# Kernel optimization log

Hardware: AMD Instinct MI355X
Metric: run time of the kernel (lower is better)

The kernel has to match this reference:

```python
import jax, jax.numpy as jnp
import numpy as np
import math

B, S, D, H, L, F = 32, 512, 512, 8, 4, 1024
TD = 4 * D  # time embedding dim
DH = D // H
SCALE = 1.0 / math.sqrt(DH)


def _ln(x, g, b):
    m = jnp.mean(x, -1, keepdims=True)
    v = jnp.var(x, -1, keepdims=True)
    return (x - m) * jax.lax.rsqrt(v + 1e-5) * g + b


def setup_inputs() -> dict:
    key = jax.random.key(0)
    ks = jax.random.split(key, 12)
    w = lambda k, shp: jax.random.normal(k, shp, dtype=jnp.float32) * 0.02
    return {
        "x": jax.random.normal(ks[0], (B, S, D), dtype=jnp.float32),
        "time": jax.random.uniform(ks[1], (B,), dtype=jnp.float32) * 1000.0,
        "time_w1": w(ks[2], (TD, D)), "time_b1": jnp.zeros((TD,), jnp.float32),
        "time_w2": w(ks[3], (TD, TD)), "time_b2": jnp.zeros((TD,), jnp.float32),
        "Wq": w(ks[4], (L, D, D)), "bq": jnp.zeros((L, D), jnp.float32),
        "Wk": w(ks[5], (L, D, D)), "bk": jnp.zeros((L, D), jnp.float32),
        "Wv": w(ks[6], (L, D, D)), "bv": jnp.zeros((L, D), jnp.float32),
        "Wo": w(ks[7], (L, D, D)), "bo": jnp.zeros((L, D), jnp.float32),
        "attn_g": jnp.ones((L, D), jnp.float32), "attn_b": jnp.zeros((L, D), jnp.float32),
        "ffn_g": jnp.ones((L, D), jnp.float32), "ffn_b": jnp.zeros((L, D), jnp.float32),
        "W1": w(ks[8], (L, 2 * F, D)), "b1": jnp.zeros((L, 2 * F), jnp.float32),
        "W2": w(ks[9], (L, D, F)), "b2": jnp.zeros((L, D), jnp.float32),
        "Wt": w(ks[10], (L, 4 * F, TD)), "bt": jnp.zeros((L, 4 * F), jnp.float32),
        "head_g": jnp.ones((D,), jnp.float32), "head_b": jnp.zeros((D,), jnp.float32),
        "Wh": w(ks[11], (D, D)), "bh": jnp.zeros((D,), jnp.float32),
    }


def _forward(x, time, time_w1, time_b1, time_w2, time_b2,
             Wq, bq, Wk, bk, Wv, bv, Wo, bo,
             attn_g, attn_b, ffn_g, ffn_b,
             W1, b1, W2, b2, Wt, bt,
             head_g, head_b, Wh, bh):
    Bsz = x.shape[0]
    # --- sinusoidal time embedding + time MLP ---
    half = D // 2
    freqs = jnp.exp(jnp.arange(half, dtype=jnp.float32) * (-math.log(10000.0) / (half - 1)))
    e = time[:, None] * freqs[None, :]
    temb = jnp.concatenate([jnp.sin(e), jnp.cos(e)], axis=-1)  # [B, D]
    temb = jax.nn.gelu(temb @ time_w1.T + time_b1, approximate=False) @ time_w2.T + time_b2  # [B, 4D]
    for i in range(L):
        # attention (prenorm; block 0 skips the norm since first_prenormalization=False)
        h = x if i == 0 else _ln(x, attn_g[i], attn_b[i])
        q = (h @ Wq[i].T + bq[i]).reshape(Bsz, S, H, DH)
        k = (h @ Wk[i].T + bk[i]).reshape(Bsz, S, H, DH)
        v = (h @ Wv[i].T + bv[i]).reshape(Bsz, S, H, DH)
        logits = jnp.einsum('bqhd,bkhd->bhqk', q, k) * SCALE
        probs = jax.nn.softmax(logits, axis=-1)
        o = jnp.einsum('bhqk,bkhd->bqhd', probs, v).reshape(Bsz, S, D)
        x = x + (o @ Wo[i].T + bo[i])
        # FFN with FiLM time conditioning and ReGLU activation
        h = _ln(x, ffn_g[i], ffn_b[i])
        h1 = h @ W1[i].T + b1[i]  # [B, S, 2F]
        tm = jax.nn.silu(temb) @ Wt[i].T + bt[i]  # [B, 4F]
        scale, shift = jnp.split(tm[:, None, :], 2, axis=-1)  # each [B, 1, 2F]
        h1 = h1 * (scale + 1.0) + shift
        a, g = jnp.split(h1, 2, axis=-1)  # ReGLU: a * relu(g)
        x = x + ((a * jax.nn.relu(g)) @ W2[i].T + b2[i])
    # head: last token -> LayerNorm -> ReLU -> Linear
    z = _ln(x[:, -1], head_g, head_b)
    return jax.nn.relu(z) @ Wh.T + bh


def reference(x, time, time_w1, time_b1, time_w2, time_b2,
              Wq, bq, Wk, bk, Wv, bv, Wo, bo,
              attn_g, attn_b, ffn_g, ffn_b,
              W1, b1, W2, b2, Wt, bt,
              head_g, head_b, Wh, bh):
    return _forward(x, time, time_w1, time_b1, time_w2, time_b2,
                    Wq, bq, Wk, bk, Wv, bv, Wo, bo,
                    attn_g, attn_b, ffn_g, ffn_b,
                    W1, b1, W2, b2, Wt, bt,
                    head_g, head_b, Wh, bh)
```

## Files before the change

### kernel.cpp

```cpp
#include <hip/hip_runtime.h>
#include <math.h>

typedef __bf16 bf16_t;
typedef __bf16 bf16x8 __attribute__((ext_vector_type(8)));
typedef float f32x4 __attribute__((ext_vector_type(4)));

__device__ __forceinline__ void gload_lds16(const void* g, void* l) {
    __builtin_amdgcn_global_load_lds(
        (const __attribute__((address_space(1))) void*)g,
        (__attribute__((address_space(3))) void*)l, 16, 0, 0);
}

__global__ void k_f2b(const float* __restrict__ in, bf16_t* __restrict__ out, int n8) {
    int idx = blockIdx.x * 256 + threadIdx.x;
    if (idx >= n8) return;
    const float* p = in + (size_t)idx * 8;
    bf16x8 r;
#pragma unroll
    for (int j = 0; j < 8; j++) r[j] = (bf16_t)p[j];
    *(bf16x8*)(out + (size_t)idx * 8) = r;
}

__global__ void k_f2b_s(const float* __restrict__ in, bf16_t* __restrict__ out,
                        int seg8, int dstride8) {
    int idx = blockIdx.x * 256 + threadIdx.x;
    int seg = idx / seg8, rem = idx - seg * seg8;
    const float* p = in + (size_t)idx * 8;
    bf16x8 r;
#pragma unroll
    for (int j = 0; j < 8; j++) r[j] = (bf16_t)p[j];
    *(bf16x8*)(out + ((size_t)seg * dstride8 + rem) * 8) = r;
}

__global__ void k_time_embed(const float* __restrict__ time, float* __restrict__ temb0) {
    int b = blockIdx.x;
    int j = threadIdx.x;
    float f = __expf((float)j * -0.036118981458730134f);
    float e = time[b] * f;
    temb0[(size_t)b * 512 + j] = sinf(e);
    temb0[(size_t)b * 512 + 256 + j] = cosf(e);
}

template<bool DO_NORM>
__global__ void k_ln(const float* __restrict__ x, const float* __restrict__ g,
                     const float* __restrict__ b, bf16_t* __restrict__ out) {
    int row = blockIdx.x * 4 + (threadIdx.x >> 6);
    int lane = threadIdx.x & 63;
    const float* xr = x + (size_t)row * 512 + lane * 8;
    float4 v0 = *(const float4*)xr;
    float4 v1 = *(const float4*)(xr + 4);
    float vals[8] = {v0.x, v0.y, v0.z, v0.w, v1.x, v1.y, v1.z, v1.w};
    bf16x8 r;
    if (DO_NORM) {
        float s = 0.f, sq = 0.f;
#pragma unroll
        for (int j = 0; j < 8; j++) { s += vals[j]; sq += vals[j] * vals[j]; }
#pragma unroll
        for (int m = 1; m < 64; m <<= 1) { s += __shfl_xor(s, m, 64); sq += __shfl_xor(sq, m, 64); }
        float mean = s * (1.0f / 512.0f);
        float var = sq * (1.0f / 512.0f) - mean * mean;
        float rstd = rsqrtf(var + 1e-5f);
        float4 g0 = *(const float4*)(g + lane * 8);
        float4 g1 = *(const float4*)(g + lane * 8 + 4);
        float4 b0 = *(const float4*)(b + lane * 8);
        float4 b1 = *(const float4*)(b + lane * 8 + 4);
        float gs[8] = {g0.x, g0.y, g0.z, g0.w, g1.x, g1.y, g1.z, g1.w};
        float bs[8] = {b0.x, b0.y, b0.z, b0.w, b1.x, b1.y, b1.z, b1.w};
#pragma unroll
        for (int j = 0; j < 8; j++) r[j] = (bf16_t)((vals[j] - mean) * rstd * gs[j] + bs[j]);
    } else {
#pragma unroll
        for (int j = 0; j < 8; j++) r[j] = (bf16_t)vals[j];
    }
    *(bf16x8*)(out + (size_t)row * 512 + lane * 8) = r;
}

__global__ void k_head_prep(const float* __restrict__ x, const float* __restrict__ g,
                            const float* __restrict__ b, float* __restrict__ z) {
    int row = blockIdx.x * 4 + (threadIdx.x >> 6);
    int lane = threadIdx.x & 63;
    const float* xr = x + ((size_t)row * 512 + 511) * 512 + lane * 8;
    float4 v0 = *(const float4*)xr;
    float4 v1 = *(const float4*)(xr + 4);
    float vals[8] = {v0.x, v0.y, v0.z, v0.w, v1.x, v1.y, v1.z, v1.w};
    float s = 0.f, sq = 0.f;
#pragma unroll
    for (int j = 0; j < 8; j++) { s += vals[j]; sq += vals[j] * vals[j]; }
#pragma unroll
    for (int m = 1; m < 64; m <<= 1) { s += __shfl_xor(s, m, 64); sq += __shfl_xor(sq, m, 64); }
    float mean = s * (1.0f / 512.0f);
    float var = sq * (1.0f / 512.0f) - mean * mean;
    float rstd = rsqrtf(var + 1e-5f);
    float o[8];
#pragma unroll
    for (int j = 0; j < 8; j++) {
        float gv = g[lane * 8 + j], bv = b[lane * 8 + j];
        o[j] = fmaxf((vals[j] - mean) * rstd * gv + bv, 0.0f);
    }
    float* zr = z + (size_t)row * 512 + lane * 8;
    *(float4*)zr = make_float4(o[0], o[1], o[2], o[3]);
    *(float4*)(zr + 4) = make_float4(o[4], o[5], o[6], o[7]);
}

template<int ACT, int K, bool OUTB>
__global__ __launch_bounds__(256, 2)
void k_gemm_tm(const float* __restrict__ A, const float* __restrict__ W,
               const float* __restrict__ bias, void* __restrict__ outp, int N) {
    __shared__ float Asm[32][516];
    const int t = threadIdx.x;
    const int kq = t & 7, rw = (t >> 3) & 7, bh = t >> 6;
    const int n0 = blockIdx.x * 32;
    float acc[4][8] = {};
    for (int k0 = 0; k0 < K; k0 += 512) {
        __syncthreads();
#pragma unroll
        for (int i = 0; i < 16; i++) {
            int fid = t + i * 256;
            int row = fid >> 7, cc = (fid & 127) << 2;
            *(float4*)&Asm[row][cc] = *(const float4*)&A[(size_t)row * K + k0 + cc];
        }
        __syncthreads();
#pragma unroll 4
        for (int j = 0; j < 16; j++) {
            int kk = kq * 4 + j * 32;
            float4 w4[4];
#pragma unroll
            for (int r = 0; r < 4; r++)
                w4[r] = *(const float4*)&W[(size_t)(n0 + rw + r * 8) * K + k0 + kk];
#pragma unroll
            for (int b = 0; b < 8; b++) {
                float4 a4 = *(const float4*)&Asm[bh * 8 + b][kk];
#pragma unroll
                for (int r = 0; r < 4; r++)
                    acc[r][b] += a4.x * w4[r].x + a4.y * w4[r].y + a4.z * w4[r].z + a4.w * w4[r].w;
            }
        }
    }
#pragma unroll
    for (int m = 1; m < 8; m <<= 1)
#pragma unroll
        for (int r = 0; r < 4; r++)
#pragma unroll
            for (int b = 0; b < 8; b++)
                acc[r][b] += __shfl_xor(acc[r][b], m, 64);
    if (kq == 0) {
#pragma unroll
        for (int r = 0; r < 4; r++) {
            int n = n0 + rw + r * 8;
            float bv = bias[n];
#pragma unroll
            for (int b = 0; b < 8; b++) {
                float v = acc[r][b] + bv;
                if (ACT == 1) v = 0.5f * v * (1.0f + erff(v * 0.70710678118654752f));
                if (ACT == 2) v = v / (1.0f + __expf(-v));
                if (OUTB) ((bf16_t*)outp)[(size_t)(bh * 8 + b) * N + n] = (bf16_t)v;
                else      ((float*)outp)[(size_t)(bh * 8 + b) * N + n] = v;
            }
        }
    }
}

__global__ void k_fill_tmt(const float* __restrict__ bt, float* __restrict__ tm_t) {
    int i = blockIdx.x * 256 + threadIdx.x;
    tm_t[i] = bt[i >> 5];
}

__global__ __launch_bounds__(256, 4)
void k_gemm_wt(const float* __restrict__ Wt, const bf16_t* __restrict__ t2s_b,
               float* __restrict__ tm_t) {
    __shared__ __align__(16) bf16_t Abuf[64 * 64];
    __shared__ __align__(16) bf16_t Bbuf[32 * 64];
    const int tid = threadIdx.x;
    const int m0 = blockIdx.x * 64;
    const int k0 = blockIdx.y * 512;
    const int lane = tid & 63, wave = tid >> 6;
    const int arow = tid >> 2, aseg = tid & 3;
    const int brow = tid >> 3, bseg = tid & 7;
    const int aswz = (arow & 7) << 4;
    const char* Bg = (const char*)t2s_b + (size_t)brow * 4096 + ((bseg * 16) ^ ((brow & 7) << 4));
    char* BbL = (char*)Bbuf + tid * 16;
    const float* Ar0 = Wt + (size_t)(m0 + arow) * 2048 + k0 + aseg * 16;
    f32x4 acc[2] = {};
    for (int kk0 = 0; kk0 < 512; kk0 += 64) {
        float4 a4[4];
#pragma unroll
        for (int i = 0; i < 4; i++) a4[i] = *(const float4*)(Ar0 + kk0 + i * 4);
        __syncthreads();
        gload_lds16(Bg + (size_t)(k0 + kk0) * 2, BbL);
        bf16x8 c0, c1;
#pragma unroll
        for (int i = 0; i < 4; i++) {
            const float* af = (const float*)&a4[i];
#pragma unroll
            for (int j = 0; j < 4; j++) {
                if (i < 2) c0[i * 4 + j] = (bf16_t)af[j];
                else       c1[(i - 2) * 4 + j] = (bf16_t)af[j];
            }
        }
        int base = arow * 128 + aseg * 32;
        *(bf16x8*)((char*)Abuf + (base ^ aswz)) = c0;
        *(bf16x8*)((char*)Abuf + ((base + 16) ^ aswz)) = c1;
        __syncthreads();
#pragma unroll
        for (int kk = 0; kk < 2; kk++) {
            int ar = wave * 16 + (lane & 15);
            bf16x8 af = *(const bf16x8*)((const char*)Abuf + ar * 128 +
                        ((kk * 64 + (lane >> 4) * 16) ^ ((ar & 7) << 4)));
#pragma unroll
            for (int j = 0; j < 2; j++) {
                int br = j * 16 + (lane & 15);
                bf16x8 bfr = *(const bf16x8*)((const char*)Bbuf + br * 128 +
                             ((kk * 64 + (lane >> 4) * 16) ^ ((br & 7) << 4)));
                acc[j] = __builtin_amdgcn_mfma_f32_16x16x32_bf16(af, bfr, acc[j], 0, 0, 0);
            }
        }
    }
#pragma unroll
    for (int j = 0; j < 2; j++)
#pragma unroll
        for (int r = 0; r < 4; r++) {
            int mrow = m0 + wave * 16 + (lane >> 4) * 4 + r;
            atomicAdd(&tm_t[(size_t)mrow * 32 + j * 16 + (lane & 15)], acc[j][r]);
        }
}

enum { EPI_QKV = 0, EPI_RESID = 1, EPI_FILMGLU = 2 };

template<int EPI, int K, int NBY>
__global__ __launch_bounds__(256, 4)
void k_gemm_bt(const bf16_t* __restrict__ A, const bf16_t* __restrict__ W,
               const float* __restrict__ bias, const float* __restrict__ bias2,
               const float* __restrict__ bias3,
               void* __restrict__ out0, void* __restrict__ out1, void* __restrict__ out2,
               const float* __restrict__ tm) {
    __shared__ __align__(16) bf16_t Abuf[128 * 64];
    __shared__ __align__(16) bf16_t Bbuf[128 * 64];
    const int tid = threadIdx.x;
    const int cpx = gridDim.x >> 3;
    const int wg = (blockIdx.x & 7) * cpx + (blockIdx.x >> 3);
    const int bx = wg / NBY;
    const int by = wg - bx * NBY;
    const int m0 = bx * 128;
    const int lane = tid & 63;
    const int wave = tid >> 6;
    const int wr = (wave >> 1) * 64, wc = (wave & 1) * 64;

    const int srow = tid >> 3;
    const int goff = ((tid & 7) * 16) ^ ((srow & 7) << 4);
    const char* Ag = (const char*)A;
    const char* Wg = (const char*)W;
    char* AbL = (char*)Abuf + tid * 16;
    char* BbL = (char*)Bbuf + tid * 16;
    int growB[4];
#pragma unroll
    for (int i = 0; i < 4; i++) {
        int r = srow + i * 32;
        if (EPI == EPI_FILMGLU) {
            int half = (r >> 5) & 1;
            int base = by * 64 + (r >> 6) * 32 + (r & 31);
            growB[i] = half * 1024 + base;
        } else {
            growB[i] = by * 128 + r;
        }
    }

    f32x4 acc[4][4] = {};
    for (int k0 = 0; k0 < K * 2; k0 += 128) {
        __syncthreads();
#pragma unroll
        for (int i = 0; i < 4; i++) {
            gload_lds16(Ag + (size_t)(m0 + srow + i * 32) * (K * 2) + k0 + goff, AbL + i * 4096);
            gload_lds16(Wg + (size_t)growB[i] * (K * 2) + k0 + goff, BbL + i * 4096);
        }
        __syncthreads();
#pragma unroll
        for (int kk = 0; kk < 2; kk++) {
            bf16x8 af[4], bfr[4];
#pragma unroll
            for (int i = 0; i < 4; i++) {
                int ar = wr + i * 16 + (lane & 15);
                af[i] = *(const bf16x8*)((const char*)Abuf + ar * 128 +
                         ((kk * 64 + (lane >> 4) * 16) ^ ((ar & 7) << 4)));
                int br = wc + i * 16 + (lane & 15);
                bfr[i] = *(const bf16x8*)((const char*)Bbuf + br * 128 +
                         ((kk * 64 + (lane >> 4) * 16) ^ ((br & 7) << 4)));
            }
#pragma unroll
            for (int i = 0; i < 4; i++)
#pragma unroll
                for (int j = 0; j < 4; j++)
                    acc[i][j] = __builtin_amdgcn_mfma_f32_16x16x32_bf16(af[i], bfr[j], acc[i][j], 0, 0, 0);
        }
    }

    const int b = m0 >> 9;
    if (EPI == EPI_QKV) {
        const int which = by >> 2;
        bf16_t* op = (bf16_t*)(which == 0 ? out0 : which == 1 ? out1 : out2);
        const float* bp = which == 0 ? bias : which == 1 ? bias2 : bias3;
#pragma unroll
        for (int i = 0; i < 4; i++) {
#pragma unroll
            for (int r = 0; r < 4; r++) {
                int s = (m0 + wr + i * 16 + (lane >> 4) * 4 + r) & 511;
#pragma unroll
                for (int j = 0; j < 4; j++) {
                    int c = (by & 3) * 128 + wc + j * 16 + (lane & 15);
                    float v = acc[i][j][r] + bp[c];
                    int h = c >> 6, dh = c & 63;
                    op[(((size_t)b * 8 + h) * 512 + s) * 64 + dh] = (bf16_t)v;
                }
            }
        }
    } else if (EPI == EPI_RESID) {
        float* op = (float*)out0;
        const float* rs = (const float*)out1;
#pragma unroll
        for (int i = 0; i < 4; i++) {
#pragma unroll
            for (int r = 0; r < 4; r++) {
                int row = m0 + wr + i * 16 + (lane >> 4) * 4 + r;
#pragma unroll
                for (int j = 0; j < 4; j++) {
                    int col = by * 128 + wc + j * 16 + (lane & 15);
                    size_t idx = (size_t)row * 512 + col;
                    op[idx] = rs[idx] + acc[i][j][r] + bias[col];
                }
            }
        }
    } else {
        bf16_t* op = (bf16_t*)out0;
#pragma unroll
        for (int i = 0; i < 4; i++) {
#pragma unroll
            for (int r = 0; r < 4; r++) {
                int row = m0 + wr + i * 16 + (lane >> 4) * 4 + r;
#pragma unroll
                for (int jj = 0; jj < 2; jj++) {
                    int colA = by * 64 + (wave & 1) * 32 + jj * 16 + (lane & 15);
                    float av = acc[i][jj][r] + bias[colA];
                    float gv = acc[i][jj + 2][r] + bias[1024 + colA];
                    float sa = tm[(size_t)colA * 32 + b];
                    float ha = tm[(size_t)(2048 + colA) * 32 + b];
                    float sg = tm[(size_t)(1024 + colA) * 32 + b];
                    float hg = tm[(size_t)(3072 + colA) * 32 + b];
                    av = av * (1.0f + sa) + ha;
                    gv = gv * (1.0f + sg) + hg;
                    op[(size_t)row * 1024 + colA] = (bf16_t)(av * fmaxf(gv, 0.0f));
                }
            }
        }
    }
}

__global__ __launch_bounds__(256, 2)
void k_attn(const bf16_t* __restrict__ q, const bf16_t* __restrict__ k,
            const bf16_t* __restrict__ v, bf16_t* __restrict__ o) {
    __shared__ bf16_t q_lds[64][72];
    __shared__ bf16_t k_lds[64][72];
    __shared__ bf16_t vt_lds[64 * 72];
    __shared__ bf16_t p_lds[64][72];
    const int tid = threadIdx.x;
    const int lane = tid & 63;
    const int wave = tid >> 6;
    const int qt = blockIdx.x;
    const int bh = blockIdx.y;
    const bf16_t* qb = q + ((size_t)bh * 512 + qt * 64) * 64;
    const bf16_t* kb = k + (size_t)bh * 512 * 64;
    const bf16_t* vb = v + (size_t)bh * 512 * 64;
    const int sr = tid >> 2;
    const int sc = (tid & 3) * 16;
    {
        bf16x8 a0 = *(const bf16x8*)(qb + sr * 64 + sc);
        bf16x8 a1 = *(const bf16x8*)(qb + sr * 64 + sc + 8);
        bf16x8 ra, rb;
#pragma unroll
        for (int j = 0; j < 8; j++) {
            ra[j] = (bf16_t)((float)a0[j] * 0.125f);
            rb[j] = (bf16_t)((float)a1[j] * 0.125f);
        }
        *(bf16x8*)&q_lds[sr][sc] = ra;
        *(bf16x8*)&q_lds[sr][sc + 8] = rb;
    }
    bf16x8 kr0, kr1, vr0, vr1;
    {
        const bf16_t* ks = kb + (size_t)sr * 64 + sc;
        const bf16_t* vs = vb + (size_t)sr * 64 + sc;
        kr0 = *(const bf16x8*)ks; kr1 = *(const bf16x8*)(ks + 8);
        vr0 = *(const bf16x8*)vs; vr1 = *(const bf16x8*)(vs + 8);
    }
    float mrow[4], lrow[4];
    f32x4 oacc[4] = {};
#pragma unroll
    for (int r = 0; r < 4; r++) { mrow[r] = -1e30f; lrow[r] = 0.f; }
    const int swz0 = ((sc >> 3) & 7) << 4;
    const int swz1 = (((sc + 8) >> 3) & 7) << 4;
    for (int kt = 0; kt < 8; kt++) {
        __syncthreads();
        {
            *(bf16x8*)&k_lds[sr][sc] = kr0;
            *(bf16x8*)&k_lds[sr][sc + 8] = kr1;
            char* vbase = (char*)vt_lds;
            int so0 = (sr * 2) ^ swz0;
            int so1 = (sr * 2) ^ swz1;
#pragma unroll
            for (int j = 0; j < 8; j++) {
                *(bf16_t*)(vbase + (sc + j) * 144 + so0) = vr0[j];
                *(bf16_t*)(vbase + (sc + 8 + j) * 144 + so1) = vr1[j];
            }
        }
        __syncthreads();
        if (kt < 7) {
            const bf16_t* ks = kb + ((size_t)(kt + 1) * 64 + sr) * 64 + sc;
            const bf16_t* vs = vb + ((size_t)(kt + 1) * 64 + sr) * 64 + sc;
            kr0 = *(const bf16x8*)ks; kr1 = *(const bf16x8*)(ks + 8);
            vr0 = *(const bf16x8*)vs; vr1 = *(const bf16x8*)(vs + 8);
        }
        f32x4 sacc[4] = {};
#pragma unroll
        for (int kk = 0; kk < 2; kk++) {
            bf16x8 aq = *(const bf16x8*)&q_lds[wave * 16 + (lane & 15)][kk * 32 + (lane >> 4) * 8];
#pragma unroll
            for (int c = 0; c < 4; c++) {
                bf16x8 bk8 = *(const bf16x8*)&k_lds[c * 16 + (lane & 15)][kk * 32 + (lane >> 4) * 8];
                sacc[c] = __builtin_amdgcn_mfma_f32_16x16x32_bf16(aq, bk8, sacc[c], 0, 0, 0);
            }
        }
#pragma unroll
        for (int r = 0; r < 4; r++) {
            float mx = fmaxf(fmaxf(sacc[0][r], sacc[1][r]), fmaxf(sacc[2][r], sacc[3][r]));
#pragma unroll
            for (int m = 1; m < 16; m <<= 1) mx = fmaxf(mx, __shfl_xor(mx, m, 64));
            float newm = fmaxf(mrow[r], mx);
            float fsc = __expf(mrow[r] - newm);
            mrow[r] = newm;
            float p0 = __expf(sacc[0][r] - newm);
            float p1 = __expf(sacc[1][r] - newm);
            float p2 = __expf(sacc[2][r] - newm);
            float p3 = __expf(sacc[3][r] - newm);
            float ps = p0 + p1 + p2 + p3;
#pragma unroll
            for (int m = 1; m < 16; m <<= 1) ps += __shfl_xor(ps, m, 64);
            lrow[r] = lrow[r] * fsc + ps;
#pragma unroll
            for (int c = 0; c < 4; c++) oacc[c][r] *= fsc;
            int qrow = wave * 16 + (lane >> 4) * 4 + r;
            p_lds[qrow][(lane & 15)] = (bf16_t)p0;
            p_lds[qrow][16 + (lane & 15)] = (bf16_t)p1;
            p_lds[qrow][32 + (lane & 15)] = (bf16_t)p2;
            p_lds[qrow][48 + (lane & 15)] = (bf16_t)p3;
        }
#pragma unroll
        for (int kk = 0; kk < 2; kk++) {
            bf16x8 ap = *(const bf16x8*)&p_lds[wave * 16 + (lane & 15)][kk * 32 + (lane >> 4) * 8];
#pragma unroll
            for (int c = 0; c < 4; c++) {
                int d0 = c * 16 + (lane & 15);
                int xo = ((d0 >> 3) & 7) << 4;
                bf16x8 bv8 = *(const bf16x8*)((const char*)vt_lds + d0 * 144 +
                              ((kk * 64 + (lane >> 4) * 16) ^ xo));
                oacc[c] = __builtin_amdgcn_mfma_f32_16x16x32_bf16(ap, bv8, oacc[c], 0, 0, 0);
            }
        }
    }
    const int b = bh >> 3, h = bh & 7;
#pragma unroll
    for (int r = 0; r < 4; r++) {
        int s = qt * 64 + wave * 16 + (lane >> 4) * 4 + r;
        float inv = 1.0f / lrow[r];
#pragma unroll
        for (int c = 0; c < 4; c++) {
            o[((size_t)b * 512 + s) * 512 + h * 64 + c * 16 + (lane & 15)] = (bf16_t)(oacc[c][r] * inv);
        }
    }
}

extern "C" void kernel_launch(void* const* d_in, const int* in_sizes, int n_in,
                              void* d_out, int out_size, void* d_ws, size_t ws_size,
                              hipStream_t stream) {
    const float* x_in   = (const float*)d_in[0];
    const float* time_in= (const float*)d_in[1];
    const float* tw1    = (const float*)d_in[2];
    const float* tb1    = (const float*)d_in[3];
    const float* tw2    = (const float*)d_in[4];
    const float* tb2    = (const float*)d_in[5];
    const float* Wq     = (const float*)d_in[6];
    const float* bq     = (const float*)d_in[7];
    const float* Wk     = (const float*)d_in[8];
    const float* bk     = (const float*)d_in[9];
    const float* Wv     = (const float*)d_in[10];
    const float* bv     = (const float*)d_in[11];
    const float* Wo     = (const float*)d_in[12];
    const float* bo     = (const float*)d_in[13];
    const float* attn_g = (const float*)d_in[14];
    const float* attn_b = (const float*)d_in[15];
    const float* ffn_g  = (const float*)d_in[16];
    const float* ffn_b  = (const float*)d_in[17];
    const float* W1     = (const float*)d_in[18];
    const float* b1     = (const float*)d_in[19];
    const float* W2     = (const float*)d_in[20];
    const float* b2     = (const float*)d_in[21];
    const float* Wt     = (const float*)d_in[22];
    const float* bt     = (const float*)d_in[23];
    const float* head_g = (const float*)d_in[24];
    const float* head_b = (const float*)d_in[25];
    const float* Wh     = (const float*)d_in[26];
    const float* bh     = (const float*)d_in[27];

    size_t off = 0;
    auto alloc = [&](size_t bytes) {
        void* r = (char*)d_ws + off;
        off += (bytes + 255) & ~(size_t)255;
        return r;
    };
    bf16_t* wqkv_b = (bf16_t*)alloc((size_t)4 * 3 * 512 * 512 * 2);
    bf16_t* wo_b   = (bf16_t*)alloc((size_t)4 * 512 * 512 * 2);
    bf16_t* w1_b   = (bf16_t*)alloc((size_t)4 * 2048 * 512 * 2);
    bf16_t* w2_b   = (bf16_t*)alloc((size_t)4 * 512 * 1024 * 2);
    float*  x_ws   = (float*)alloc((size_t)16384 * 512 * 4);
    bf16_t* h_b    = (bf16_t*)alloc((size_t)16384 * 512 * 2);
    bf16_t* q_b    = (bf16_t*)alloc((size_t)16384 * 512 * 2);
    bf16_t* k_b    = (bf16_t*)alloc((size_t)16384 * 512 * 2);
    bf16_t* v_b    = (bf16_t*)alloc((size_t)16384 * 512 * 2);
    bf16_t* o_b    = (bf16_t*)alloc((size_t)16384 * 512 * 2);
    bf16_t* act_b  = (bf16_t*)alloc((size_t)16384 * 1024 * 2);
    float*  temb0  = (float*)alloc((size_t)32 * 512 * 4);
    float*  t1     = (float*)alloc((size_t)32 * 2048 * 4);
    bf16_t* t2s_b  = (bf16_t*)alloc((size_t)32 * 2048 * 2);
    float*  tm_t   = (float*)alloc((size_t)16384 * 32 * 4);
    float*  z      = (float*)alloc((size_t)32 * 512 * 4);

    k_f2b_s<<<512, 256, 0, stream>>>(Wq, wqkv_b,          32768, 98304);
    k_f2b_s<<<512, 256, 0, stream>>>(Wk, wqkv_b + 262144, 32768, 98304);
    k_f2b_s<<<512, 256, 0, stream>>>(Wv, wqkv_b + 524288, 32768, 98304);
    k_f2b<<<512, 256, 0, stream>>>(Wo, wo_b, 131072);
    k_f2b<<<2048, 256, 0, stream>>>(W1, w1_b, 524288);
    k_f2b<<<1024, 256, 0, stream>>>(W2, w2_b, 262144);

    k_time_embed<<<32, 256, 0, stream>>>(time_in, temb0);
    k_gemm_tm<1, 512, false><<<64, 256, 0, stream>>>(temb0, tw1, tb1, t1, 2048);
    k_gemm_tm<2, 2048, true><<<64, 256, 0, stream>>>(t1, tw2, tb2, t2s_b, 2048);
    k_fill_tmt<<<2048, 256, 0, stream>>>(bt, tm_t);
    k_gemm_wt<<<dim3(256, 4), 256, 0, stream>>>(Wt, t2s_b, tm_t);

    for (int l = 0; l < 4; l++) {
        if (l == 0)
            k_ln<false><<<4096, 256, 0, stream>>>(x_in, nullptr, nullptr, h_b);
        else
            k_ln<true><<<4096, 256, 0, stream>>>(x_ws, attn_g + l * 512, attn_b + l * 512, h_b);

        k_gemm_bt<EPI_QKV, 512, 12><<<1536, 256, 0, stream>>>(
            h_b, wqkv_b + (size_t)l * 786432,
            bq + l * 512, bk + l * 512, bv + l * 512,
            q_b, k_b, v_b, nullptr);

        k_attn<<<dim3(8, 256), 256, 0, stream>>>(q_b, k_b, v_b, o_b);

        k_gemm_bt<EPI_RESID, 512, 4><<<512, 256, 0, stream>>>(
            o_b, wo_b + (size_t)l * 262144,
            bo + l * 512, nullptr, nullptr,
            x_ws, (void*)(l == 0 ? x_in : x_ws), nullptr, nullptr);

        k_ln<true><<<4096, 256, 0, stream>>>(x_ws, ffn_g + l * 512, ffn_b + l * 512, h_b);

        k_gemm_bt<EPI_FILMGLU, 512, 16><<<2048, 256, 0, stream>>>(
            h_b, w1_b + (size_t)l * 1048576,
            b1 + l * 2048, nullptr, nullptr,
            act_b, nullptr, nullptr, tm_t + (size_t)l * 4096 * 32);

        k_gemm_bt<EPI_RESID, 1024, 4><<<512, 256, 0, stream>>>(
            act_b, w2_b + (size_t)l * 524288,
            b2 + l * 512, nullptr, nullptr,
            x_ws, x_ws, nullptr, nullptr);
    }

    k_head_prep<<<8, 256, 0, stream>>>(x_ws, head_g, head_b, z);
    k_gemm_tm<0, 512, false><<<16, 256, 0, stream>>>(z, Wh, bh, (float*)d_out, 512);
}
```

Measured before the change: 1.155 ms.

## Replace GEMM with 8-wave 256x128 double-buffered ping-pong pipelined kernel

```diff
diff --git a/kernel.cpp b/kernel.cpp
--- a/kernel.cpp
+++ b/kernel.cpp
@@ -227,129 +227,153 @@
 enum { EPI_QKV = 0, EPI_RESID = 1, EPI_FILMGLU = 2 };
 
 template<int EPI, int K, int NBY>
-__global__ __launch_bounds__(256, 4)
-void k_gemm_bt(const bf16_t* __restrict__ A, const bf16_t* __restrict__ W,
-               const float* __restrict__ bias, const float* __restrict__ bias2,
-               const float* __restrict__ bias3,
-               void* __restrict__ out0, void* __restrict__ out1, void* __restrict__ out2,
-               const float* __restrict__ tm) {
-    __shared__ __align__(16) bf16_t Abuf[128 * 64];
-    __shared__ __align__(16) bf16_t Bbuf[128 * 64];
+__global__ __launch_bounds__(512, 2)
+void k_gemm8p(const bf16_t* __restrict__ A, const bf16_t* __restrict__ W,
+              const float* __restrict__ bias, const float* __restrict__ bias2,
+              const float* __restrict__ bias3,
+              void* __restrict__ out0, void* __restrict__ out1, void* __restrict__ out2,
+              const float* __restrict__ tm) {
+    __shared__ __align__(16) bf16_t Ab[2][256 * 64];
+    __shared__ __align__(16) bf16_t Bb[2][128 * 64];
     const int tid = threadIdx.x;
-    const int cpx = gridDim.x >> 3;
-    const int wg = (blockIdx.x & 7) * cpx + (blockIdx.x >> 3);
-    const int bx = wg / NBY;
-    const int by = wg - bx * NBY;
-    const int m0 = bx * 128;
+    const int cpx = (NBY * 64) >> 3;
+    const int wg = ((int)blockIdx.x & 7) * cpx + ((int)blockIdx.x >> 3);
+    const int bx = wg / NBY, by = wg - bx * NBY;
+    const int m0 = bx * 256;
     const int lane = tid & 63;
-    const int wave = tid >> 6;
-    const int wr = (wave >> 1) * 64, wc = (wave & 1) * 64;
+    const int wid = tid >> 6;
+    const int wrM = wid >> 1, wrN = wid & 1;
 
     const int srow = tid >> 3;
     const int goff = ((tid & 7) * 16) ^ ((srow & 7) << 4);
     const char* Ag = (const char*)A;
     const char* Wg = (const char*)W;
-    char* AbL = (char*)Abuf + tid * 16;
-    char* BbL = (char*)Bbuf + tid * 16;
-    int growB[4];
-#pragma unroll
-    for (int i = 0; i < 4; i++) {
-        int r = srow + i * 32;
+    int growB[2];
+#pragma unroll
+    for (int rnd = 0; rnd < 2; rnd++) {
+        int r = srow + rnd * 64;
         if (EPI == EPI_FILMGLU) {
-            int half = (r >> 5) & 1;
-            int base = by * 64 + (r >> 6) * 32 + (r & 31);
-            growB[i] = half * 1024 + base;
+            int sub = r & 63;
+            growB[rnd] = (sub >> 5) * 1024 + by * 64 + (r >> 6) * 32 + (sub & 31);
         } else {
-            growB[i] = by * 128 + r;
-        }
-    }
+            growB[rnd] = by * 128 + r;
+        }
+    }
+
+    auto stageHalf = [&](int buf, int kt, int half) {
+        const int k0 = kt * 128;
+        char* adst = (char*)Ab[buf] + tid * 16 + half * 16384;
+#pragma unroll
+        for (int rr = 0; rr < 2; rr++) {
+            int row = m0 + srow + (half * 2 + rr) * 64;
+            gload_lds16(Ag + (size_t)row * (K * 2) + k0 + goff, adst + rr * 8192);
+        }
+        gload_lds16(Wg + (size_t)growB[half] * (K * 2) + k0 + goff,
+                    (char*)Bb[buf] + tid * 16 + half * 8192);
+    };
 
     f32x4 acc[4][4] = {};
-    for (int k0 = 0; k0 < K * 2; k0 += 128) {
-        __syncthreads();
-#pragma unroll
-        for (int i = 0; i < 4; i++) {
-            gload_lds16(Ag + (size_t)(m0 + srow + i * 32) * (K * 2) + k0 + goff, AbL + i * 4096);
-            gload_lds16(Wg + (size_t)growB[i] * (K * 2) + k0 + goff, BbL + i * 4096);
-        }
-        __syncthreads();
-#pragma unroll
-        for (int kk = 0; kk < 2; kk++) {
-            bf16x8 af[4], bfr[4];
-#pragma unroll
-            for (int i = 0; i < 4; i++) {
-                int ar = wr + i * 16 + (lane & 15);
-                af[i] = *(const bf16x8*)((const char*)Abuf + ar * 128 +
-                         ((kk * 64 + (lane >> 4) * 16) ^ ((ar & 7) << 4)));
-                int br = wc + i * 16 + (lane & 15);
-                bfr[i] = *(const bf16x8*)((const char*)Bbuf + br * 128 +
-                         ((kk * 64 + (lane >> 4) * 16) ^ ((br & 7) << 4)));
-            }
-#pragma unroll
-            for (int i = 0; i < 4; i++)
-#pragma unroll
-                for (int j = 0; j < 4; j++)
-                    acc[i][j] = __builtin_amdgcn_mfma_f32_16x16x32_bf16(af[i], bfr[j], acc[i][j], 0, 0, 0);
-        }
-    }
-
-    const int b = m0 >> 9;
+    bf16x8 af[4];
+
+    stageHalf(0, 0, 0);
+    stageHalf(0, 0, 1);
+    asm volatile("s_waitcnt vmcnt(0)" ::: "memory");
+    __builtin_amdgcn_s_barrier();
+
+    const int NITER = K / 128;
+    for (int j = 0; j < NITER; ++j) {
+#pragma unroll
+        for (int p = 0; p < 8; ++p) {
+            const int buf = p >> 2;
+            const int kkh = (p >> 1) & 1;
+            const int nig = p & 1;
+            if (nig == 0) {
+#pragma unroll
+                for (int mi = 0; mi < 4; mi++) {
+                    int ar = wrM * 64 + mi * 16 + (lane & 15);
+                    af[mi] = *(const bf16x8*)((const char*)Ab[buf] + ar * 128 +
+                              ((kkh * 64 + (lane >> 4) * 16) ^ ((ar & 7) << 4)));
+                }
+            }
+            bf16x8 bf0, bf1;
+            {
+                int br0 = wrN * 64 + nig * 32 + (lane & 15);
+                bf0 = *(const bf16x8*)((const char*)Bb[buf] + br0 * 128 +
+                       ((kkh * 64 + (lane >> 4) * 16) ^ ((br0 & 7) << 4)));
+                int br1 = br0 + 16;
+                bf1 = *(const bf16x8*)((const char*)Bb[buf] + br1 * 128 +
+                       ((kkh * 64 + (lane >> 4) * 16) ^ ((br1 & 7) << 4)));
+            }
+            if (p == 0) stageHalf(1, 2 * j + 1, 0);
+            if (p == 1) stageHalf(1, 2 * j + 1, 1);
+            if (p == 4 && j + 1 < NITER) stageHalf(0, 2 * j + 2, 0);
+            if (p == 5 && j + 1 < NITER) stageHalf(0, 2 * j + 2, 1);
+            if (p == 3 || p == 7) asm volatile("s_waitcnt vmcnt(0)" ::: "memory");
+            __builtin_amdgcn_s_barrier();
+            __builtin_amdgcn_s_setprio(1);
+#pragma unroll
+            for (int mi = 0; mi < 4; mi++) {
+                acc[mi][nig * 2]     = __builtin_amdgcn_mfma_f32_16x16x32_bf16(af[mi], bf0, acc[mi][nig * 2], 0, 0, 0);
+                acc[mi][nig * 2 + 1] = __builtin_amdgcn_mfma_f32_16x16x32_bf16(af[mi], bf1, acc[mi][nig * 2 + 1], 0, 0, 0);
+            }
+            __builtin_amdgcn_s_setprio(0);
+            __builtin_amdgcn_s_barrier();
+        }
+    }
+
+    const int bb = m0 >> 9;
     if (EPI == EPI_QKV) {
         const int which = by >> 2;
         bf16_t* op = (bf16_t*)(which == 0 ? out0 : which == 1 ? out1 : out2);
         const float* bp = which == 0 ? bias : which == 1 ? bias2 : bias3;
 #pragma unroll
-        for (int i = 0; i < 4; i++) {
-#pragma unroll
-            for (int r = 0; r < 4; r++) {
-                int s = (m0 + wr + i * 16 + (lane >> 4) * 4 + r) & 511;
-#pragma unroll
-                for (int j = 0; j < 4; j++) {
-                    int c = (by & 3) * 128 + wc + j * 16 + (lane & 15);
-                    float v = acc[i][j][r] + bp[c];
-                    int h = c >> 6, dh = c & 63;
-                    op[(((size_t)b * 8 + h) * 512 + s) * 64 + dh] = (bf16_t)v;
+        for (int mi = 0; mi < 4; mi++)
+#pragma unroll
+            for (int rr = 0; rr < 4; rr++) {
+                int s = (m0 + wrM * 64 + mi * 16 + (lane >> 4) * 4 + rr) & 511;
+#pragma unroll
+                for (int ni = 0; ni < 4; ni++) {
+                    int c = (by & 3) * 128 + wrN * 64 + ni * 16 + (lane & 15);
+                    float v = acc[mi][ni][rr] + bp[c];
+                    op[(((size_t)bb * 8 + (c >> 6)) * 512 + s) * 64 + (c & 63)] = (bf16_t)v;
                 }
             }
-        }
     } else if (EPI == EPI_RESID) {
         float* op = (float*)out0;
         const float* rs = (const float*)out1;
 #pragma unroll
-        for (int i = 0; i < 4; i++) {
-#pragma unroll
-            for (int r = 0; r < 4; r++) {
-                int row = m0 + wr + i * 16 + (lane >> 4) * 4 + r;
-#pragma unroll
-                for (int j = 0; j < 4; j++) {
-                    int col = by * 128 + wc + j * 16 + (lane & 15);
+        for (int mi = 0; mi < 4; mi++)
+#pragma unroll
+            for (int rr = 0; rr < 4; rr++) {
+                int row = m0 + wrM * 64 + mi * 16 + (lane >> 4) * 4 + rr;
+#pragma unroll
+                for (int ni = 0; ni < 4; ni++) {
+                    int col = by * 128 + wrN * 64 + ni * 16 + (lane & 15);
                     size_t idx = (size_t)row * 512 + col;
-                    op[idx] = rs[idx] + acc[i][j][r] + bias[col];
+                    op[idx] = rs[idx] + acc[mi][ni][rr] + bias[col];
                 }
             }
-        }
     } else {
         bf16_t* op = (bf16_t*)out0;
 #pragma unroll
-        for (int i = 0; i < 4; i++) {
-#pragma unroll
-            for (int r = 0; r < 4; r++) {
-                int row = m0 + wr + i * 16 + (lane >> 4) * 4 + r;
-#pragma unroll
-                for (int jj = 0; jj < 2; jj++) {
-                    int colA = by * 64 + (wave & 1) * 32 + jj * 16 + (lane & 15);
-                    float av = acc[i][jj][r] + bias[colA];
-                    float gv = acc[i][jj + 2][r] + bias[1024 + colA];
-                    float sa = tm[(size_t)colA * 32 + b];
-                    float ha = tm[(size_t)(2048 + colA) * 32 + b];
-                    float sg = tm[(size_t)(1024 + colA) * 32 + b];
-                    float hg = tm[(size_t)(3072 + colA) * 32 + b];
+        for (int mi = 0; mi < 4; mi++)
+#pragma unroll
+            for (int rr = 0; rr < 4; rr++) {
+                int row = m0 + wrM * 64 + mi * 16 + (lane >> 4) * 4 + rr;
+#pragma unroll
+                for (int ni = 0; ni < 2; ni++) {
+                    int colA = by * 64 + wrN * 32 + ni * 16 + (lane & 15);
+                    float av = acc[mi][ni][rr] + bias[colA];
+                    float gv = acc[mi][ni + 2][rr] + bias[1024 + colA];
+                    float sa = tm[(size_t)colA * 32 + bb];
+                    float ha = tm[(size_t)(2048 + colA) * 32 + bb];
+                    float sg = tm[(size_t)(1024 + colA) * 32 + bb];
+                    float hg = tm[(size_t)(3072 + colA) * 32 + bb];
                     av = av * (1.0f + sa) + ha;
                     gv = gv * (1.0f + sg) + hg;
                     op[(size_t)row * 1024 + colA] = (bf16_t)(av * fmaxf(gv, 0.0f));
                 }
             }
-        }
     }
 }
 
@@ -549,26 +573,26 @@
         else
             k_ln<true><<<4096, 256, 0, stream>>>(x_ws, attn_g + l * 512, attn_b + l * 512, h_b);
 
-        k_gemm_bt<EPI_QKV, 512, 12><<<1536, 256, 0, stream>>>(
+        k_gemm8p<EPI_QKV, 512, 12><<<768, 512, 0, stream>>>(
             h_b, wqkv_b + (size_t)l * 786432,
             bq + l * 512, bk + l * 512, bv + l * 512,
             q_b, k_b, v_b, nullptr);
 
         k_attn<<<dim3(8, 256), 256, 0, stream>>>(q_b, k_b, v_b, o_b);
 
-        k_gemm_bt<EPI_RESID, 512, 4><<<512, 256, 0, stream>>>(
+        k_gemm8p<EPI_RESID, 512, 4><<<256, 512, 0, stream>>>(
             o_b, wo_b + (size_t)l * 262144,
             bo + l * 512, nullptr, nullptr,
             x_ws, (void*)(l == 0 ? x_in : x_ws), nullptr, nullptr);
 
         k_ln<true><<<4096, 256, 0, stream>>>(x_ws, ffn_g + l * 512, ffn_b + l * 512, h_b);
 
-        k_gemm_bt<EPI_FILMGLU, 512, 16><<<2048, 256, 0, stream>>>(
+        k_gemm8p<EPI_FILMGLU, 512, 16><<<1024, 512, 0, stream>>>(
             h_b, w1_b + (size_t)l * 1048576,
             b1 + l * 2048, nullptr, nullptr,
             act_b, nullptr, nullptr, tm_t + (size_t)l * 4096 * 32);
 
-        k_gemm_bt<EPI_RESID, 1024, 4><<<512, 256, 0, stream>>>(
+        k_gemm8p<EPI_RESID, 1024, 4><<<256, 512, 0, stream>>>(
             act_b, w2_b + (size_t)l * 524288,
             b2 + l * 512, nullptr, nullptr,
             x_ws, x_ws, nullptr, nullptr);
```

Result: slower. 1.329 ms (+15.1%).

## Load GEMM operands directly from global into registers, dropping LDS staging

Applied to the files above, without the earlier changes.

```diff
diff --git a/kernel.cpp b/kernel.cpp
--- a/kernel.cpp
+++ b/kernel.cpp
@@ -227,14 +227,12 @@
 enum { EPI_QKV = 0, EPI_RESID = 1, EPI_FILMGLU = 2 };
 
 template<int EPI, int K, int NBY>
-__global__ __launch_bounds__(256, 4)
+__global__ __launch_bounds__(256, 3)
 void k_gemm_bt(const bf16_t* __restrict__ A, const bf16_t* __restrict__ W,
                const float* __restrict__ bias, const float* __restrict__ bias2,
                const float* __restrict__ bias3,
                void* __restrict__ out0, void* __restrict__ out1, void* __restrict__ out2,
                const float* __restrict__ tm) {
-    __shared__ __align__(16) bf16_t Abuf[128 * 64];
-    __shared__ __align__(16) bf16_t Bbuf[128 * 64];
     const int tid = threadIdx.x;
     const int cpx = gridDim.x >> 3;
     const int wg = (blockIdx.x & 7) * cpx + (blockIdx.x >> 3);
@@ -244,52 +242,54 @@
     const int lane = tid & 63;
     const int wave = tid >> 6;
     const int wr = (wave >> 1) * 64, wc = (wave & 1) * 64;
-
-    const int srow = tid >> 3;
-    const int goff = ((tid & 7) * 16) ^ ((srow & 7) << 4);
-    const char* Ag = (const char*)A;
-    const char* Wg = (const char*)W;
-    char* AbL = (char*)Abuf + tid * 16;
-    char* BbL = (char*)Bbuf + tid * 16;
-    int growB[4];
-#pragma unroll
-    for (int i = 0; i < 4; i++) {
-        int r = srow + i * 32;
-        if (EPI == EPI_FILMGLU) {
-            int half = (r >> 5) & 1;
-            int base = by * 64 + (r >> 6) * 32 + (r & 31);
-            growB[i] = half * 1024 + base;
+    const int lrow = lane & 15;
+    const int kboff = (lane >> 4) * 16;
+
+    const char* Abase[4];
+    const char* Bbase[4];
+#pragma unroll
+    for (int i = 0; i < 4; i++)
+        Abase[i] = (const char*)A + (size_t)(m0 + wr + i * 16 + lrow) * (K * 2) + kboff;
+#pragma unroll
+    for (int j = 0; j < 4; j++) {
+        int row;
+        if (EPI == EPI_FILMGLU)
+            row = (j >> 1) * 1024 + by * 64 + (wave & 1) * 32 + (j & 1) * 16 + lrow;
+        else
+            row = by * 128 + wc + j * 16 + lrow;
+        Bbase[j] = (const char*)W + (size_t)row * (K * 2) + kboff;
+    }
+
+    bf16x8 a0[4], b0[4], a1[4], b1[4];
+#pragma unroll
+    for (int i = 0; i < 4; i++) { a0[i] = *(const bf16x8*)(Abase[i]); b0[i] = *(const bf16x8*)(Bbase[i]); }
+
+    f32x4 acc[4][4] = {};
+    const int NH = K / 32;
+#pragma unroll
+    for (int h = 0; h < NH; ++h) {
+        if (h + 1 < NH) {
+            const int koff = (h + 1) * 64;
+            if ((h & 1) == 0) {
+#pragma unroll
+                for (int i = 0; i < 4; i++) { a1[i] = *(const bf16x8*)(Abase[i] + koff); b1[i] = *(const bf16x8*)(Bbase[i] + koff); }
+            } else {
+#pragma unroll
+                for (int i = 0; i < 4; i++) { a0[i] = *(const bf16x8*)(Abase[i] + koff); b0[i] = *(const bf16x8*)(Bbase[i] + koff); }
+            }
+        }
+        if ((h & 1) == 0) {
+#pragma unroll
+            for (int i = 0; i < 4; i++)
+#pragma unroll
+                for (int j = 0; j < 4; j++)
+                    acc[i][j] = __builtin_amdgcn_mfma_f32_16x16x32_bf16(a0[i], b0[j], acc[i][j], 0, 0, 0);
         } else {
-            growB[i] = by * 128 + r;
-        }
-    }
-
-    f32x4 acc[4][4] = {};
-    for (int k0 = 0; k0 < K * 2; k0 += 128) {
-        __syncthreads();
-#pragma unroll
-        for (int i = 0; i < 4; i++) {
-            gload_lds16(Ag + (size_t)(m0 + srow + i * 32) * (K * 2) + k0 + goff, AbL + i * 4096);
-            gload_lds16(Wg + (size_t)growB[i] * (K * 2) + k0 + goff, BbL + i * 4096);
-        }
-        __syncthreads();
-#pragma unroll
-        for (int kk = 0; kk < 2; kk++) {
-            bf16x8 af[4], bfr[4];
-#pragma unroll
-            for (int i = 0; i < 4; i++) {
-                int ar = wr + i * 16 + (lane & 15);
-                af[i] = *(const bf16x8*)((const char*)Abuf + ar * 128 +
-                         ((kk * 64 + (lane >> 4) * 16) ^ ((ar & 7) << 4)));
-                int br = wc + i * 16 + (lane & 15);
-                bfr[i] = *(const bf16x8*)((const char*)Bbuf + br * 128 +
-                         ((kk * 64 + (lane >> 4) * 16) ^ ((br & 7) << 4)));
-            }
 #pragma unroll
             for (int i = 0; i < 4; i++)
 #pragma unroll
                 for (int j = 0; j < 4; j++)
-                    acc[i][j] = __builtin_amdgcn_mfma_f32_16x16x32_bf16(af[i], bfr[j], acc[i][j], 0, 0, 0);
+                    acc[i][j] = __builtin_amdgcn_mfma_f32_16x16x32_bf16(a1[i], b1[j], acc[i][j], 0, 0, 0);
         }
     }
 
@@ -307,8 +307,8 @@
                 for (int j = 0; j < 4; j++) {
                     int c = (by & 3) * 128 + wc + j * 16 + (lane & 15);
                     float v = acc[i][j][r] + bp[c];
-                    int h = c >> 6, dh = c & 63;
-                    op[(((size_t)b * 8 + h) * 512 + s) * 64 + dh] = (bf16_t)v;
+                    int h2 = c >> 6, dh = c & 63;
+                    op[(((size_t)b * 8 + h2) * 512 + s) * 64 + dh] = (bf16_t)v;
                 }
             }
         }
```

New measurement: 1.946 ms. 1.69x slower.

## Store residual stream in bf16 and swizzle attention grid for XCD locality

Applied to the files above, without the earlier changes.

```diff
diff --git a/kernel.cpp b/kernel.cpp
--- a/kernel.cpp
+++ b/kernel.cpp
@@ -41,15 +41,23 @@
     temb0[(size_t)b * 512 + 256 + j] = cosf(e);
 }
 
-template<bool DO_NORM>
-__global__ void k_ln(const float* __restrict__ x, const float* __restrict__ g,
+template<bool DO_NORM, bool IN32>
+__global__ void k_ln(const void* __restrict__ xp, const float* __restrict__ g,
                      const float* __restrict__ b, bf16_t* __restrict__ out) {
     int row = blockIdx.x * 4 + (threadIdx.x >> 6);
     int lane = threadIdx.x & 63;
-    const float* xr = x + (size_t)row * 512 + lane * 8;
-    float4 v0 = *(const float4*)xr;
-    float4 v1 = *(const float4*)(xr + 4);
-    float vals[8] = {v0.x, v0.y, v0.z, v0.w, v1.x, v1.y, v1.z, v1.w};
+    float vals[8];
+    if (IN32) {
+        const float* xr = (const float*)xp + (size_t)row * 512 + lane * 8;
+        float4 v0 = *(const float4*)xr;
+        float4 v1 = *(const float4*)(xr + 4);
+        vals[0] = v0.x; vals[1] = v0.y; vals[2] = v0.z; vals[3] = v0.w;
+        vals[4] = v1.x; vals[5] = v1.y; vals[6] = v1.z; vals[7] = v1.w;
+    } else {
+        bf16x8 xv = *(const bf16x8*)((const bf16_t*)xp + (size_t)row * 512 + lane * 8);
+#pragma unroll
+        for (int j = 0; j < 8; j++) vals[j] = (float)xv[j];
+    }
     bf16x8 r;
     if (DO_NORM) {
         float s = 0.f, sq = 0.f;
@@ -75,14 +83,14 @@
     *(bf16x8*)(out + (size_t)row * 512 + lane * 8) = r;
 }
 
-__global__ void k_head_prep(const float* __restrict__ x, const float* __restrict__ g,
+__global__ void k_head_prep(const bf16_t* __restrict__ x, const float* __restrict__ g,
                             const float* __restrict__ b, float* __restrict__ z) {
     int row = blockIdx.x * 4 + (threadIdx.x >> 6);
     int lane = threadIdx.x & 63;
-    const float* xr = x + ((size_t)row * 512 + 511) * 512 + lane * 8;
-    float4 v0 = *(const float4*)xr;
-    float4 v1 = *(const float4*)(xr + 4);
-    float vals[8] = {v0.x, v0.y, v0.z, v0.w, v1.x, v1.y, v1.z, v1.w};
+    bf16x8 xv = *(const bf16x8*)(x + ((size_t)row * 512 + 511) * 512 + lane * 8);
+    float vals[8];
+#pragma unroll
+    for (int j = 0; j < 8; j++) vals[j] = (float)xv[j];
     float s = 0.f, sq = 0.f;
 #pragma unroll
     for (int j = 0; j < 8; j++) { s += vals[j]; sq += vals[j] * vals[j]; }
@@ -226,12 +234,12 @@
 
 enum { EPI_QKV = 0, EPI_RESID = 1, EPI_FILMGLU = 2 };
 
-template<int EPI, int K, int NBY>
+template<int EPI, int K, int NBY, bool RS32>
 __global__ __launch_bounds__(256, 4)
 void k_gemm_bt(const bf16_t* __restrict__ A, const bf16_t* __restrict__ W,
                const float* __restrict__ bias, const float* __restrict__ bias2,
                const float* __restrict__ bias3,
-               void* __restrict__ out0, void* __restrict__ out1, void* __restrict__ out2,
+               void* __restrict__ out0, const void* __restrict__ rsp, void* __restrict__ out2,
                const float* __restrict__ tm) {
     __shared__ __align__(16) bf16_t Abuf[128 * 64];
     __shared__ __align__(16) bf16_t Bbuf[128 * 64];
@@ -296,7 +304,7 @@
     const int b = m0 >> 9;
     if (EPI == EPI_QKV) {
         const int which = by >> 2;
-        bf16_t* op = (bf16_t*)(which == 0 ? out0 : which == 1 ? out1 : out2);
+        bf16_t* op = (bf16_t*)(which == 0 ? out0 : which == 1 ? (void*)rsp : out2);
         const float* bp = which == 0 ? bias : which == 1 ? bias2 : bias3;
 #pragma unroll
         for (int i = 0; i < 4; i++) {
@@ -313,8 +321,7 @@
             }
         }
     } else if (EPI == EPI_RESID) {
-        float* op = (float*)out0;
-        const float* rs = (const float*)out1;
+        bf16_t* op = (bf16_t*)out0;
 #pragma unroll
         for (int i = 0; i < 4; i++) {
 #pragma unroll
@@ -324,7 +331,8 @@
                 for (int j = 0; j < 4; j++) {
                     int col = by * 128 + wc + j * 16 + (lane & 15);
                     size_t idx = (size_t)row * 512 + col;
-                    op[idx] = rs[idx] + acc[i][j][r] + bias[col];
+                    float rsv = RS32 ? ((const float*)rsp)[idx] : (float)((const bf16_t*)rsp)[idx];
+                    op[idx] = (bf16_t)(rsv + acc[i][j][r] + bias[col]);
                 }
             }
         }
@@ -363,8 +371,10 @@
     const int tid = threadIdx.x;
     const int lane = tid & 63;
     const int wave = tid >> 6;
-    const int qt = blockIdx.x;
-    const int bh = blockIdx.y;
+    const int cpx = gridDim.x >> 3;
+    const int wg = ((int)blockIdx.x & 7) * cpx + ((int)blockIdx.x >> 3);
+    const int bh = wg >> 3;
+    const int qt = wg & 7;
     const bf16_t* qb = q + ((size_t)bh * 512 + qt * 64) * 64;
     const bf16_t* kb = k + (size_t)bh * 512 * 64;
     const bf16_t* vb = v + (size_t)bh * 512 * 64;
@@ -517,7 +527,7 @@
     bf16_t* wo_b   = (bf16_t*)alloc((size_t)4 * 512 * 512 * 2);
     bf16_t* w1_b   = (bf16_t*)alloc((size_t)4 * 2048 * 512 * 2);
     bf16_t* w2_b   = (bf16_t*)alloc((size_t)4 * 512 * 1024 * 2);
-    float*  x_ws   = (float*)alloc((size_t)16384 * 512 * 4);
+    bf16_t* x_ws   = (bf16_t*)alloc((size_t)16384 * 512 * 2);
     bf16_t* h_b    = (bf16_t*)alloc((size_t)16384 * 512 * 2);
     bf16_t* q_b    = (bf16_t*)alloc((size_t)16384 * 512 * 2);
     bf16_t* k_b    = (bf16_t*)alloc((size_t)16384 * 512 * 2);
@@ -545,30 +555,36 @@
 
     for (int l = 0; l < 4; l++) {
         if (l == 0)
-            k_ln<false><<<4096, 256, 0, stream>>>(x_in, nullptr, nullptr, h_b);
+            k_ln<false, true><<<4096, 256, 0, stream>>>(x_in, nullptr, nullptr, h_b);
         else
-            k_ln<true><<<4096, 256, 0, stream>>>(x_ws, attn_g + l * 512, attn_b + l * 512, h_b);
-
-        k_gemm_bt<EPI_QKV, 512, 12><<<1536, 256, 0, stream>>>(
+            k_ln<true, false><<<4096, 256, 0, stream>>>(x_ws, attn_g + l * 512, attn_b + l * 512, h_b);
+
+        k_gemm_bt<EPI_QKV, 512, 12, false><<<1536, 256, 0, stream>>>(
             h_b, wqkv_b + (size_t)l * 786432,
             bq + l * 512, bk + l * 512, bv + l * 512,
             q_b, k_b, v_b, nullptr);
 
-        k_attn<<<dim3(8, 256), 256, 0, stream>>>(q_b, k_b, v_b, o_b);
-
-        k_gemm_bt<EPI_RESID, 512, 4><<<512, 256, 0, stream>>>(
-            o_b, wo_b + (size_t)l * 262144,
-            bo + l * 512, nullptr, nullptr,
-            x_ws, (void*)(l == 0 ? x_in : x_ws), nullptr, nullptr);
-
-        k_ln<true><<<4096, 256, 0, stream>>>(x_ws, ffn_g + l * 512, ffn_b + l * 512, h_b);
-
-        k_gemm_bt<EPI_FILMGLU, 512, 16><<<2048, 256, 0, stream>>>(
+        k_attn<<<2048, 256, 0, stream>>>(q_b, k_b, v_b, o_b);
+
+        if (l == 0)
+            k_gemm_bt<EPI_RESID, 512, 4, true><<<512, 256, 0, stream>>>(
+                o_b, wo_b + (size_t)l * 262144,
+                bo + l * 512, nullptr, nullptr,
+                x_ws, x_in, nullptr, nullptr);
+        else
+            k_gemm_bt<EPI_RESID, 512, 4, false><<<512, 256, 0, stream>>>(
+                o_b, wo_b + (size_t)l * 262144,
+                bo + l * 512, nullptr, nullptr,
+                x_ws, x_ws, nullptr, nullptr);
+
+        k_ln<true, false><<<4096, 256, 0, stream>>>(x_ws, ffn_g + l * 512, ffn_b + l * 512, h_b);
+
+        k_gemm_bt<EPI_FILMGLU, 512, 16, false><<<2048, 256, 0, stream>>>(
             h_b, w1_b + (size_t)l * 1048576,
             b1 + l * 2048, nullptr, nullptr,
             act_b, nullptr, nullptr, tm_t + (size_t)l * 4096 * 32);
 
-        k_gemm_bt<EPI_RESID, 1024, 4><<<512, 256, 0, stream>>>(
+        k_gemm_bt<EPI_RESID, 1024, 4, false><<<512, 256, 0, stream>>>(
             act_b, w2_b + (size_t)l * 524288,
             b2 + l * 512, nullptr, nullptr,
             x_ws, x_ws, nullptr, nullptr);
```

After: 1.081 ms. -6.4%, faster.
